# Optimization experiments

Hardware: AMD Instinct MI355X
Metric: run time of the kernel (lower is better)

Reference implementation:

```python
import jax, jax.numpy as jnp
import numpy as np

B, N, D, H = 8, 1024, 512, 512  # batch, nodes/graph, input dim, hidden/output dim
NEG_SLOPE = 0.2


def _gatv2_layer(x, src, dst, Wl, bl, Wr, br, a, bias, nseg):
    """PyG GATv2Conv (heads=1, add_self_loops=False, eval mode -> no dropout).
    message j->i: alpha_ij = softmax_i( a . leaky_relu(xl[j] + xr[i]) ); out[i] = sum_j alpha_ij * xl[j] + bias
    """
    xl = x @ Wl + bl              # [nseg, H] source transform
    xr = x @ Wr + br              # [nseg, H] target transform
    e = jax.nn.leaky_relu(xl[src] + xr[dst], NEG_SLOPE) @ a  # [E] raw scores
    m = jax.lax.stop_gradient(jax.ops.segment_max(e, dst, num_segments=nseg))
    ex = jnp.exp(e - m[dst])
    s = jax.ops.segment_sum(ex, dst, num_segments=nseg)
    alpha = ex / s[dst]                                       # segment softmax over incoming edges
    out = jax.ops.segment_sum(alpha[:, None] * xl[src], dst, num_segments=nseg)
    return out + bias


def setup_inputs() -> dict:
    key = jax.random.key(0)
    rng = np.random.RandomState(0)
    # random per-graph adjacency, avg degree ~16; block-diagonal edge extraction
    adj_np = (rng.rand(B, N, N) < (16.0 / N))
    srcs, dsts = [], []
    for b in range(B):  # matches torch.nonzero(big_adj).t(): row=src, col=dst
        r, c = np.nonzero(adj_np[b])
        srcs.append(r + b * N)
        dsts.append(c + b * N)
    edge_index = jnp.asarray(np.stack([np.concatenate(srcs), np.concatenate(dsts)]).astype(np.int32))

    ks = jax.random.split(key, 32)
    def lin(k, fi, fo):
        return (jax.random.normal(k, (fi, fo), jnp.float32) / np.sqrt(fi)).astype(jnp.float32)
    inp = {
        "batch_graph": jax.random.normal(ks[0], (B, N, D), jnp.float32),
        "adj": jnp.asarray(adj_np.astype(np.float32)),
        "edge_index": edge_index,
    }
    dims = [(D, H), (H, H), (H, H)]
    for i, (fi, fo) in enumerate(dims, start=1):
        k = jax.random.split(ks[i], 6)
        inp[f"Wl{i}"] = lin(k[0], fi, fo)
        inp[f"bl{i}"] = jnp.zeros((fo,), jnp.float32)
        inp[f"Wr{i}"] = lin(k[1], fi, fo)
        inp[f"br{i}"] = jnp.zeros((fo,), jnp.float32)
        inp[f"a{i}"] = (jax.random.normal(k[2], (fo,), jnp.float32) / np.sqrt(fo)).astype(jnp.float32)
        inp[f"bias{i}"] = jnp.zeros((fo,), jnp.float32)
    return inp


def reference(batch_graph, adj, edge_index,
              Wl1, bl1, Wr1, br1, a1, bias1,
              Wl2, bl2, Wr2, br2, a2, bias2,
              Wl3, bl3, Wr3, br3, a3, bias3):
    b, n, d = batch_graph.shape
    nseg = b * n
    x = batch_graph.reshape(nseg, d)
    src, dst = edge_index[0], edge_index[1]
    x = _gatv2_layer(x, src, dst, Wl1, bl1, Wr1, br1, a1, bias1, nseg)  # graph_norm = Identity
    x = _gatv2_layer(x, src, dst, Wl2, bl2, Wr2, br2, a2, bias2, nseg)
    x = _gatv2_layer(x, src, dst, Wl3, bl3, Wr3, br3, a3, bias3, nseg)
    return x.reshape(b, n, -1)
```

## Files before the change

### kernel.cpp

```cpp
#include <hip/hip_runtime.h>
#include <math.h>

#define MTOT 8192
#define HD   512

typedef __attribute__((ext_vector_type(8))) short bf16x8;
typedef __attribute__((ext_vector_type(4))) float floatx4;

__device__ inline unsigned short f2bf(float f) {
    unsigned int u = __float_as_uint(f);
    unsigned int r = (u + 0x7FFFu + ((u >> 16) & 1u)) >> 16;
    return (unsigned short)r;
}
__device__ inline float bf2f(unsigned short h) {
    return __uint_as_float(((unsigned int)h) << 16);
}


__global__ void count_deg(const int* __restrict__ dst, int* __restrict__ deg, int E) {
    int i = blockIdx.x * 256 + threadIdx.x;
    if (i < E) atomicAdd(&deg[dst[i]], 1);
}

__global__ __launch_bounds__(1024) void scan_offsets(const int* __restrict__ deg,
                                                     int* __restrict__ offs,
                                                     int* __restrict__ cursor) {
    __shared__ int part[1024];
    int tid = threadIdx.x;
    int base = tid * 8;
    int v[8]; int s = 0;
    #pragma unroll
    for (int i = 0; i < 8; ++i) { v[i] = deg[base + i]; s += v[i]; }
    part[tid] = s;
    __syncthreads();
    for (int off = 1; off < 1024; off <<= 1) {
        int t = (tid >= off) ? part[tid - off] : 0;
        __syncthreads();
        part[tid] += t;
        __syncthreads();
    }
    int run = (tid == 0) ? 0 : part[tid - 1];
    #pragma unroll
    for (int i = 0; i < 8; ++i) {
        offs[base + i] = run;
        cursor[base + i] = run;
        run += v[i];
    }
    if (tid == 1023) offs[MTOT] = run;
}

__global__ void scatter_edges(const int* __restrict__ src, const int* __restrict__ dst,
                              int* __restrict__ cursor, int* __restrict__ csr_src, int E) {
    int i = blockIdx.x * 256 + threadIdx.x;
    if (i < E) {
        int p = atomicAdd(&cursor[dst[i]], 1);
        csr_src[p] = src[i];
    }
}


__global__ __launch_bounds__(256) void prep_convert(
    const float* __restrict__ W0, const float* __restrict__ W1,
    const float* __restrict__ W2, const float* __restrict__ W3,
    const float* __restrict__ W4, const float* __restrict__ W5,
    unsigned short* __restrict__ wtbase,
    const float* __restrict__ X,
    unsigned short* __restrict__ Ahi, unsigned short* __restrict__ Alo,
    int* __restrict__ deg)
{
    int z = blockIdx.z;
    if (z == 7) {
        if (blockIdx.x == 0 && blockIdx.y == 0)
            for (int i = threadIdx.x; i < MTOT; i += 256) deg[i] = 0;
        return;
    }
    if (z == 6) {
        int bid = blockIdx.x * 16 + blockIdx.y;
        int t0 = bid * 256 + threadIdx.x;
        #pragma unroll
        for (int it = 0; it < 16; ++it) {
            int i = (t0 + it * 65536) * 4;
            float4 vv = *(const float4*)(X + i);
            ushort4 h, l;
            h.x = f2bf(vv.x); l.x = f2bf(vv.x - bf2f(h.x));
            h.y = f2bf(vv.y); l.y = f2bf(vv.y - bf2f(h.y));
            h.z = f2bf(vv.z); l.z = f2bf(vv.z - bf2f(h.z));
            h.w = f2bf(vv.w); l.w = f2bf(vv.w - bf2f(h.w));
            *(ushort4*)(Ahi + i) = h;
            *(ushort4*)(Alo + i) = l;
        }
        return;
    }
    const float* W = (z == 0) ? W0 : (z == 1) ? W1 : (z == 2) ? W2
                   : (z == 3) ? W3 : (z == 4) ? W4 : W5;
    int L = z >> 1, lr = z & 1;
    const size_t SZ = (size_t)HD * HD;
    unsigned short* Whi = wtbase + (L * 4 + lr * 2) * SZ;
    unsigned short* Wlo = Whi + SZ;

    __shared__ float t[32][33];
    int bx = blockIdx.x * 32;
    int by = blockIdx.y * 32;
    int tx = threadIdx.x & 31, ty = threadIdx.x >> 5;
    for (int i = ty; i < 32; i += 8)
        t[i][tx] = W[(size_t)(by + i) * HD + bx + tx];
    __syncthreads();
    for (int i = ty; i < 32; i += 8) {
        float vv = t[tx][i];
        unsigned short h = f2bf(vv);
        unsigned short l = f2bf(vv - bf2f(h));
        Whi[(size_t)(bx + i) * HD + by + tx] = h;
        Wlo[(size_t)(bx + i) * HD + by + tx] = l;
    }
}


__global__ __launch_bounds__(256) void gemm_mfma_dual(
    const unsigned short* __restrict__ Ahi, const unsigned short* __restrict__ Alo,
    const unsigned short* __restrict__ Bhi_l, const unsigned short* __restrict__ Blo_l,
    const unsigned short* __restrict__ Bhi_r, const unsigned short* __restrict__ Blo_r,
    const float* __restrict__ bias_l, const float* __restrict__ bias_r,
    float* __restrict__ Cl, float* __restrict__ Cr,
    const float* __restrict__ avec,
    float* __restrict__ slpart, float* __restrict__ srpart)
{
    const unsigned short* Bhi = blockIdx.z ? Bhi_r : Bhi_l;
    const unsigned short* Blo = blockIdx.z ? Blo_r : Blo_l;
    const float* bias         = blockIdx.z ? bias_r : bias_l;
    float* C                  = blockIdx.z ? Cr : Cl;
    float* spart              = blockIdx.z ? srpart : slpart;

    __shared__ __align__(16) unsigned short lds[4 * 128 * 32];

    int tid = threadIdx.x;
    int wave = tid >> 6, lane = tid & 63;
    int bm = blockIdx.y * 128, bn = blockIdx.x * 128;

    const unsigned short* gsrc[4] = {Ahi, Alo, Bhi, Blo};
    int rowbase[4] = {bm, bm, bn, bn};

    const unsigned short* gbase =
        gsrc[wave] + (size_t)(rowbase[wave] + (lane >> 2)) * 512 + (lane & 3) * 8;

    floatx4 acc[4][4] = {};

    int wm = wave & 1, wn = wave >> 1;
    int lr = lane & 15, lq = lane >> 4;

    for (int k0 = 0; k0 < 512; k0 += 32) {
        const unsigned short* g = gbase + k0;
        #pragma unroll
        for (int rg = 0; rg < 8; ++rg) {
            __builtin_amdgcn_global_load_lds(
                (const __attribute__((address_space(1))) unsigned int*)(g + (size_t)rg * 16 * 512),
                (__attribute__((address_space(3))) unsigned int*)(&lds[wave * 4096 + rg * 512]),
                16, 0, 0);
        }
        __syncthreads();

        bf16x8 ah[4], al[4], bh[4], bl_[4];
        #pragma unroll
        for (int i = 0; i < 4; ++i) {
            int mrow = wm * 64 + i * 16 + lr;
            ah[i]  = *(const bf16x8*)&lds[0 * 4096 + mrow * 32 + lq * 8];
            al[i]  = *(const bf16x8*)&lds[1 * 4096 + mrow * 32 + lq * 8];
            int nrow = wn * 64 + i * 16 + lr;
            bh[i]  = *(const bf16x8*)&lds[2 * 4096 + nrow * 32 + lq * 8];
            bl_[i] = *(const bf16x8*)&lds[3 * 4096 + nrow * 32 + lq * 8];
        }
        #pragma unroll
        for (int i = 0; i < 4; ++i)
            #pragma unroll
            for (int j = 0; j < 4; ++j) {
                acc[i][j] = __builtin_amdgcn_mfma_f32_16x16x32_bf16(ah[i], bh[j],  acc[i][j], 0, 0, 0);
                acc[i][j] = __builtin_amdgcn_mfma_f32_16x16x32_bf16(ah[i], bl_[j], acc[i][j], 0, 0, 0);
                acc[i][j] = __builtin_amdgcn_mfma_f32_16x16x32_bf16(al[i], bh[j],  acc[i][j], 0, 0, 0);
            }
        __syncthreads();
    }

    #pragma unroll
    for (int j = 0; j < 4; ++j) {
        int n = bn + wn * 64 + j * 16 + lr;
        float bv = bias[n];
        #pragma unroll
        for (int i = 0; i < 4; ++i) {
            int mbase = bm + wm * 64 + i * 16 + lq * 4;
            #pragma unroll
            for (int r = 0; r < 4; ++r)
                C[(size_t)(mbase + r) * 512 + n] = acc[i][j][r] + bv;
        }
    }

    {
        float aj[4], bj[4];
        #pragma unroll
        for (int j = 0; j < 4; ++j) {
            int n = bn + wn * 64 + j * 16 + lr;
            aj[j] = avec[n];
            bj[j] = bias[n];
        }
        float badd = fmaf(aj[0], bj[0], fmaf(aj[1], bj[1],
                     fmaf(aj[2], bj[2], aj[3] * bj[3])));
        #pragma unroll
        for (int i = 0; i < 4; ++i) {
            #pragma unroll
            for (int r = 0; r < 4; ++r) {
                float v = fmaf(aj[0], acc[i][0][r],
                          fmaf(aj[1], acc[i][1][r],
                          fmaf(aj[2], acc[i][2][r],
                          fmaf(aj[3], acc[i][3][r], badd))));
                v += __shfl_xor(v, 1, 64);
                v += __shfl_xor(v, 2, 64);
                v += __shfl_xor(v, 4, 64);
                v += __shfl_xor(v, 8, 64);
                if (lr == 0) {
                    int row = bm + wm * 64 + i * 16 + lq * 4 + r;
                    spart[(size_t)row * 8 + blockIdx.x * 2 + wn] = v;
                }
            }
        }
    }
}


__global__ __launch_bounds__(256) void gat_online(
    const float* __restrict__ xl, const float* __restrict__ xr,
    const float* __restrict__ slpart, const float* __restrict__ srpart,
    const float* __restrict__ avec, const float* __restrict__ bias,
    const int* __restrict__ offs, const int* __restrict__ csr_src,
    float* __restrict__ out, unsigned short* __restrict__ Ohi,
    unsigned short* __restrict__ Olo, int write_fp32)
{
    int gid = blockIdx.x;
    int wv = threadIdx.x >> 6, lane = threadIdx.x & 63;
    int node = ((gid & 7) << 10) + ((gid >> 3) << 2) + wv;

    int nb = offs[node], ne = offs[node + 1];

    size_t rowoff = (size_t)node * HD + lane * 8;
    float4 r0 = *(const float4*)(xr + rowoff);
    float4 r1 = *(const float4*)(xr + rowoff + 4);
    float4 av0 = *(const float4*)(avec + lane * 8);
    float4 av1 = *(const float4*)(avec + lane * 8 + 4);

    float4 sr0 = *(const float4*)(srpart + (size_t)node * 8);
    float4 sr1 = *(const float4*)(srpart + (size_t)node * 8 + 4);
    float sr = ((sr0.x + sr0.y) + (sr0.z + sr0.w)) + ((sr1.x + sr1.y) + (sr1.z + sr1.w));

    float m = -3.0e38f, s = 0.f;
    float4 acc0 = {0.f, 0.f, 0.f, 0.f}, acc1 = {0.f, 0.f, 0.f, 0.f};

    int p = nb;
    int jnx = 0;
    float4 nx0 = {0,0,0,0}, nx1 = {0,0,0,0}, nsl0 = {0,0,0,0}, nsl1 = {0,0,0,0};
    if (p < ne) {
        int j0 = __builtin_amdgcn_readfirstlane(csr_src[p]);
        const float* xp = xl + (size_t)j0 * HD + lane * 8;
        nx0 = *(const float4*)xp;
        nx1 = *(const float4*)(xp + 4);
        nsl0 = *(const float4*)(slpart + (size_t)j0 * 8);
        nsl1 = *(const float4*)(slpart + (size_t)j0 * 8 + 4);
    }
    if (p + 1 < ne) jnx = __builtin_amdgcn_readfirstlane(csr_src[p + 1]);

    while (p < ne) {
        float4 cx0 = nx0, cx1 = nx1;
        float slj = ((nsl0.x + nsl0.y) + (nsl0.z + nsl0.w)) +
                    ((nsl1.x + nsl1.y) + (nsl1.z + nsl1.w));

        int jpre = jnx;
        if (p + 2 < ne) jnx = __builtin_amdgcn_readfirstlane(csr_src[p + 2]);
        if (p + 1 < ne) {
            const float* xp = xl + (size_t)jpre * HD + lane * 8;
            nx0 = *(const float4*)xp;
            nx1 = *(const float4*)(xp + 4);
            nsl0 = *(const float4*)(slpart + (size_t)jpre * 8);
            nsl1 = *(const float4*)(slpart + (size_t)jpre * 8 + 4);
        }

        float t, pe = 0.f;
        t = cx0.x + r0.x; pe = fmaf(av0.x, fabsf(t), pe);
        t = cx0.y + r0.y; pe = fmaf(av0.y, fabsf(t), pe);
        t = cx0.z + r0.z; pe = fmaf(av0.z, fabsf(t), pe);
        t = cx0.w + r0.w; pe = fmaf(av0.w, fabsf(t), pe);
        t = cx1.x + r1.x; pe = fmaf(av1.x, fabsf(t), pe);
        t = cx1.y + r1.y; pe = fmaf(av1.y, fabsf(t), pe);
        t = cx1.z + r1.z; pe = fmaf(av1.z, fabsf(t), pe);
        t = cx1.w + r1.w; pe = fmaf(av1.w, fabsf(t), pe);
        pe += __shfl_xor(pe, 1, 64);
        pe += __shfl_xor(pe, 2, 64);
        pe += __shfl_xor(pe, 4, 64);
        pe += __shfl_xor(pe, 8, 64);
        pe += __shfl_xor(pe, 16, 64);
        pe += __shfl_xor(pe, 32, 64);

        float e = fmaf(0.4f, pe, 0.6f * (slj + sr));

        float w;
        if (e > m) {
            float sc = __expf(m - e);
            s *= sc;
            acc0.x *= sc; acc0.y *= sc; acc0.z *= sc; acc0.w *= sc;
            acc1.x *= sc; acc1.y *= sc; acc1.z *= sc; acc1.w *= sc;
            m = e; w = 1.f;
        } else {
            w = __expf(e - m);
        }
        s += w;
        acc0.x = fmaf(w, cx0.x, acc0.x);
        acc0.y = fmaf(w, cx0.y, acc0.y);
        acc0.z = fmaf(w, cx0.z, acc0.z);
        acc0.w = fmaf(w, cx0.w, acc0.w);
        acc1.x = fmaf(w, cx1.x, acc1.x);
        acc1.y = fmaf(w, cx1.y, acc1.y);
        acc1.z = fmaf(w, cx1.z, acc1.z);
        acc1.w = fmaf(w, cx1.w, acc1.w);
        ++p;
    }

    float inv = (s > 0.f) ? 1.f / s : 0.f;
    float4 b0 = *(const float4*)(bias + lane * 8);
    float4 b1 = *(const float4*)(bias + lane * 8 + 4);
    float4 o0, o1;
    o0.x = fmaf(acc0.x, inv, b0.x); o0.y = fmaf(acc0.y, inv, b0.y);
    o0.z = fmaf(acc0.z, inv, b0.z); o0.w = fmaf(acc0.w, inv, b0.w);
    o1.x = fmaf(acc1.x, inv, b1.x); o1.y = fmaf(acc1.y, inv, b1.y);
    o1.z = fmaf(acc1.z, inv, b1.z); o1.w = fmaf(acc1.w, inv, b1.w);

    if (write_fp32) {
        *(float4*)(out + rowoff) = o0;
        *(float4*)(out + rowoff + 4) = o1;
    } else {
        ushort4 h, lo;
        h.x = f2bf(o0.x); lo.x = f2bf(o0.x - bf2f(h.x));
        h.y = f2bf(o0.y); lo.y = f2bf(o0.y - bf2f(h.y));
        h.z = f2bf(o0.z); lo.z = f2bf(o0.z - bf2f(h.z));
        h.w = f2bf(o0.w); lo.w = f2bf(o0.w - bf2f(h.w));
        *(ushort4*)(Ohi + rowoff) = h;
        *(ushort4*)(Olo + rowoff) = lo;
        h.x = f2bf(o1.x); lo.x = f2bf(o1.x - bf2f(h.x));
        h.y = f2bf(o1.y); lo.y = f2bf(o1.y - bf2f(h.y));
        h.z = f2bf(o1.z); lo.z = f2bf(o1.z - bf2f(h.z));
        h.w = f2bf(o1.w); lo.w = f2bf(o1.w - bf2f(h.w));
        *(ushort4*)(Ohi + rowoff + 4) = h;
        *(ushort4*)(Olo + rowoff + 4) = lo;
    }
}


extern "C" void kernel_launch(void* const* d_in, const int* in_sizes, int n_in,
                              void* d_out, int out_size, void* d_ws, size_t ws_size,
                              hipStream_t stream) {
    const float* x0 = (const float*)d_in[0];
    const int* eidx = (const int*)d_in[2];
    int E = in_sizes[2] / 2;
    const int* esrc = eidx;
    const int* edst = eidx + E;

    const float* Wl[3] = {(const float*)d_in[3],  (const float*)d_in[9],  (const float*)d_in[15]};
    const float* bl[3] = {(const float*)d_in[4],  (const float*)d_in[10], (const float*)d_in[16]};
    const float* Wr[3] = {(const float*)d_in[5],  (const float*)d_in[11], (const float*)d_in[17]};
    const float* br[3] = {(const float*)d_in[6],  (const float*)d_in[12], (const float*)d_in[18]};
    const float* av[3] = {(const float*)d_in[7],  (const float*)d_in[13], (const float*)d_in[19]};
    const float* bs[3] = {(const float*)d_in[8],  (const float*)d_in[14], (const float*)d_in[20]};

    char* w = (char*)d_ws;
    unsigned short* Ahi = (unsigned short*)w; w += (size_t)MTOT * HD * 2;
    unsigned short* Alo = (unsigned short*)w; w += (size_t)MTOT * HD * 2;
    unsigned short* wtbase = (unsigned short*)w; w += 12 * (size_t)HD * HD * 2;
    float* xl = (float*)w; w += (size_t)MTOT * HD * 4;
    float* xr = (float*)w; w += (size_t)MTOT * HD * 4;
    int* deg    = (int*)w;
    int* offs   = deg + MTOT;
    int* cursor = offs + MTOT + 8;
    int* csr    = cursor + MTOT;
    float* slpart = (float*)(((uintptr_t)(csr + E) + 63) & ~(uintptr_t)63);
    float* srpart = slpart + (size_t)MTOT * 8;
    const size_t SZ = (size_t)HD * HD;

    prep_convert<<<dim3(16, 16, 8), 256, 0, stream>>>(
        Wl[0], Wr[0], Wl[1], Wr[1], Wl[2], Wr[2], wtbase, x0, Ahi, Alo, deg);
    count_deg<<<(E + 255) / 256, 256, 0, stream>>>(edst, deg, E);
    scan_offsets<<<1, 1024, 0, stream>>>(deg, offs, cursor);
    scatter_edges<<<(E + 255) / 256, 256, 0, stream>>>(esrc, edst, cursor, csr, E);

    dim3 ggrid(HD / 128, MTOT / 128, 2);
    for (int L = 0; L < 3; ++L) {
        gemm_mfma_dual<<<ggrid, 256, 0, stream>>>(Ahi, Alo,
            wtbase + (L * 4 + 0) * SZ, wtbase + (L * 4 + 1) * SZ,
            wtbase + (L * 4 + 2) * SZ, wtbase + (L * 4 + 3) * SZ,
            bl[L], br[L], xl, xr, av[L], slpart, srpart);
        int last = (L == 2);
        gat_online<<<MTOT / 4, 256, 0, stream>>>(xl, xr, slpart, srpart, av[L], bs[L],
                                                 offs, csr,
                                                 last ? (float*)d_out : nullptr,
                                                 last ? nullptr : Ahi,
                                                 last ? nullptr : Alo,
                                                 last);
    }
}
```

Before: 346.6 us.

## Process four edges per iteration and drop the GEMM-epilogue score partials

The online-softmax aggregation now gathers four source rows per iteration and batches their shuffle reductions and exp calls, so more memory loads are in flight per wave. The leaky-ReLU decomposition (precomputed linear part via per-row a·x partial sums written by the GEMM epilogue) is replaced by computing leaky_relu directly per element. This removes the extra epilogue reduction and partial-sum traffic from the GEMM, at the cost of more VALU work per edge. Padding edges beyond the degree are masked with a very negative score.

```diff
diff --git a/kernel.cpp b/kernel.cpp
--- a/kernel.cpp
+++ b/kernel.cpp
@@ -120,15 +120,12 @@
     const unsigned short* __restrict__ Bhi_l, const unsigned short* __restrict__ Blo_l,
     const unsigned short* __restrict__ Bhi_r, const unsigned short* __restrict__ Blo_r,
     const float* __restrict__ bias_l, const float* __restrict__ bias_r,
-    float* __restrict__ Cl, float* __restrict__ Cr,
-    const float* __restrict__ avec,
-    float* __restrict__ slpart, float* __restrict__ srpart)
+    float* __restrict__ Cl, float* __restrict__ Cr)
 {
     const unsigned short* Bhi = blockIdx.z ? Bhi_r : Bhi_l;
     const unsigned short* Blo = blockIdx.z ? Blo_r : Blo_l;
     const float* bias         = blockIdx.z ? bias_r : bias_l;
     float* C                  = blockIdx.z ? Cr : Cl;
-    float* spart              = blockIdx.z ? srpart : slpart;
 
     __shared__ __align__(16) unsigned short lds[4 * 128 * 32];
 
@@ -191,42 +188,24 @@
                 C[(size_t)(mbase + r) * 512 + n] = acc[i][j][r] + bv;
         }
     }
-
-    {
-        float aj[4], bj[4];
-        #pragma unroll
-        for (int j = 0; j < 4; ++j) {
-            int n = bn + wn * 64 + j * 16 + lr;
-            aj[j] = avec[n];
-            bj[j] = bias[n];
-        }
-        float badd = fmaf(aj[0], bj[0], fmaf(aj[1], bj[1],
-                     fmaf(aj[2], bj[2], aj[3] * bj[3])));
-        #pragma unroll
-        for (int i = 0; i < 4; ++i) {
-            #pragma unroll
-            for (int r = 0; r < 4; ++r) {
-                float v = fmaf(aj[0], acc[i][0][r],
-                          fmaf(aj[1], acc[i][1][r],
-                          fmaf(aj[2], acc[i][2][r],
-                          fmaf(aj[3], acc[i][3][r], badd))));
-                v += __shfl_xor(v, 1, 64);
-                v += __shfl_xor(v, 2, 64);
-                v += __shfl_xor(v, 4, 64);
-                v += __shfl_xor(v, 8, 64);
-                if (lr == 0) {
-                    int row = bm + wm * 64 + i * 16 + lq * 4 + r;
-                    spart[(size_t)row * 8 + blockIdx.x * 2 + wn] = v;
-                }
-            }
-        }
-    }
-}
-
+}
+
+
+#define EDGE_DOT8(pe, xa, xb)                                                  \
+    {                                                                          \
+        float t_, l_;                                                          \
+        t_ = xa.x + r0.x; l_ = fmaf(0.4f, fabsf(t_), 0.6f * t_); pe = fmaf(av0.x, l_, pe); \
+        t_ = xa.y + r0.y; l_ = fmaf(0.4f, fabsf(t_), 0.6f * t_); pe = fmaf(av0.y, l_, pe); \
+        t_ = xa.z + r0.z; l_ = fmaf(0.4f, fabsf(t_), 0.6f * t_); pe = fmaf(av0.z, l_, pe); \
+        t_ = xa.w + r0.w; l_ = fmaf(0.4f, fabsf(t_), 0.6f * t_); pe = fmaf(av0.w, l_, pe); \
+        t_ = xb.x + r1.x; l_ = fmaf(0.4f, fabsf(t_), 0.6f * t_); pe = fmaf(av1.x, l_, pe); \
+        t_ = xb.y + r1.y; l_ = fmaf(0.4f, fabsf(t_), 0.6f * t_); pe = fmaf(av1.y, l_, pe); \
+        t_ = xb.z + r1.z; l_ = fmaf(0.4f, fabsf(t_), 0.6f * t_); pe = fmaf(av1.z, l_, pe); \
+        t_ = xb.w + r1.w; l_ = fmaf(0.4f, fabsf(t_), 0.6f * t_); pe = fmaf(av1.w, l_, pe); \
+    }
 
 __global__ __launch_bounds__(256) void gat_online(
     const float* __restrict__ xl, const float* __restrict__ xr,
-    const float* __restrict__ slpart, const float* __restrict__ srpart,
     const float* __restrict__ avec, const float* __restrict__ bias,
     const int* __restrict__ offs, const int* __restrict__ csr_src,
     float* __restrict__ out, unsigned short* __restrict__ Ohi,
@@ -244,79 +223,83 @@
     float4 av0 = *(const float4*)(avec + lane * 8);
     float4 av1 = *(const float4*)(avec + lane * 8 + 4);
 
-    float4 sr0 = *(const float4*)(srpart + (size_t)node * 8);
-    float4 sr1 = *(const float4*)(srpart + (size_t)node * 8 + 4);
-    float sr = ((sr0.x + sr0.y) + (sr0.z + sr0.w)) + ((sr1.x + sr1.y) + (sr1.z + sr1.w));
-
     float m = -3.0e38f, s = 0.f;
     float4 acc0 = {0.f, 0.f, 0.f, 0.f}, acc1 = {0.f, 0.f, 0.f, 0.f};
 
     int p = nb;
-    int jnx = 0;
-    float4 nx0 = {0,0,0,0}, nx1 = {0,0,0,0}, nsl0 = {0,0,0,0}, nsl1 = {0,0,0,0};
+    int jc0 = 0, jc1 = 0, jc2 = 0, jc3 = 0;
     if (p < ne) {
-        int j0 = __builtin_amdgcn_readfirstlane(csr_src[p]);
-        const float* xp = xl + (size_t)j0 * HD + lane * 8;
-        nx0 = *(const float4*)xp;
-        nx1 = *(const float4*)(xp + 4);
-        nsl0 = *(const float4*)(slpart + (size_t)j0 * 8);
-        nsl1 = *(const float4*)(slpart + (size_t)j0 * 8 + 4);
-    }
-    if (p + 1 < ne) jnx = __builtin_amdgcn_readfirstlane(csr_src[p + 1]);
+        jc0 = csr_src[p];
+        jc1 = (p + 1 < ne) ? csr_src[p + 1] : jc0;
+        jc2 = (p + 2 < ne) ? csr_src[p + 2] : jc0;
+        jc3 = (p + 3 < ne) ? csr_src[p + 3] : jc0;
+    }
 
     while (p < ne) {
-        float4 cx0 = nx0, cx1 = nx1;
-        float slj = ((nsl0.x + nsl0.y) + (nsl0.z + nsl0.w)) +
-                    ((nsl1.x + nsl1.y) + (nsl1.z + nsl1.w));
-
-        int jpre = jnx;
-        if (p + 2 < ne) jnx = __builtin_amdgcn_readfirstlane(csr_src[p + 2]);
-        if (p + 1 < ne) {
-            const float* xp = xl + (size_t)jpre * HD + lane * 8;
-            nx0 = *(const float4*)xp;
-            nx1 = *(const float4*)(xp + 4);
-            nsl0 = *(const float4*)(slpart + (size_t)jpre * 8);
-            nsl1 = *(const float4*)(slpart + (size_t)jpre * 8 + 4);
-        }
-
-        float t, pe = 0.f;
-        t = cx0.x + r0.x; pe = fmaf(av0.x, fabsf(t), pe);
-        t = cx0.y + r0.y; pe = fmaf(av0.y, fabsf(t), pe);
-        t = cx0.z + r0.z; pe = fmaf(av0.z, fabsf(t), pe);
-        t = cx0.w + r0.w; pe = fmaf(av0.w, fabsf(t), pe);
-        t = cx1.x + r1.x; pe = fmaf(av1.x, fabsf(t), pe);
-        t = cx1.y + r1.y; pe = fmaf(av1.y, fabsf(t), pe);
-        t = cx1.z + r1.z; pe = fmaf(av1.z, fabsf(t), pe);
-        t = cx1.w + r1.w; pe = fmaf(av1.w, fabsf(t), pe);
-        pe += __shfl_xor(pe, 1, 64);
-        pe += __shfl_xor(pe, 2, 64);
-        pe += __shfl_xor(pe, 4, 64);
-        pe += __shfl_xor(pe, 8, 64);
-        pe += __shfl_xor(pe, 16, 64);
-        pe += __shfl_xor(pe, 32, 64);
-
-        float e = fmaf(0.4f, pe, 0.6f * (slj + sr));
-
-        float w;
-        if (e > m) {
-            float sc = __expf(m - e);
+        const float* xp0 = xl + (size_t)jc0 * HD + lane * 8;
+        const float* xp1 = xl + (size_t)jc1 * HD + lane * 8;
+        const float* xp2 = xl + (size_t)jc2 * HD + lane * 8;
+        const float* xp3 = xl + (size_t)jc3 * HD + lane * 8;
+        float4 xa0 = *(const float4*)xp0, xb0 = *(const float4*)(xp0 + 4);
+        float4 xa1 = *(const float4*)xp1, xb1 = *(const float4*)(xp1 + 4);
+        float4 xa2 = *(const float4*)xp2, xb2 = *(const float4*)(xp2 + 4);
+        float4 xa3 = *(const float4*)xp3, xb3 = *(const float4*)(xp3 + 4);
+
+        bool v1 = (p + 1 < ne), v2 = (p + 2 < ne), v3 = (p + 3 < ne);
+
+        int jn0 = jc0, jn1 = jc0, jn2 = jc0, jn3 = jc0;
+        int pn = p + 4;
+        if (pn < ne) {
+            jn0 = csr_src[pn];
+            jn1 = (pn + 1 < ne) ? csr_src[pn + 1] : jn0;
+            jn2 = (pn + 2 < ne) ? csr_src[pn + 2] : jn0;
+            jn3 = (pn + 3 < ne) ? csr_src[pn + 3] : jn0;
+        }
+
+        float pe0 = 0.f, pe1 = 0.f, pe2 = 0.f, pe3 = 0.f;
+        EDGE_DOT8(pe0, xa0, xb0);
+        EDGE_DOT8(pe1, xa1, xb1);
+        EDGE_DOT8(pe2, xa2, xb2);
+        EDGE_DOT8(pe3, xa3, xb3);
+
+        #pragma unroll
+        for (int off = 1; off < 64; off <<= 1) {
+            pe0 += __shfl_xor(pe0, off, 64);
+            pe1 += __shfl_xor(pe1, off, 64);
+            pe2 += __shfl_xor(pe2, off, 64);
+            pe3 += __shfl_xor(pe3, off, 64);
+        }
+
+        float e0 = pe0;
+        float e1 = v1 ? pe1 : -3.0e38f;
+        float e2 = v2 ? pe2 : -3.0e38f;
+        float e3 = v3 ? pe3 : -3.0e38f;
+
+        float bm = fmaxf(fmaxf(e0, e1), fmaxf(e2, e3));
+        if (bm > m) {
+            float sc = __expf(m - bm);
             s *= sc;
             acc0.x *= sc; acc0.y *= sc; acc0.z *= sc; acc0.w *= sc;
             acc1.x *= sc; acc1.y *= sc; acc1.z *= sc; acc1.w *= sc;
-            m = e; w = 1.f;
-        } else {
-            w = __expf(e - m);
-        }
-        s += w;
-        acc0.x = fmaf(w, cx0.x, acc0.x);
-        acc0.y = fmaf(w, cx0.y, acc0.y);
-        acc0.z = fmaf(w, cx0.z, acc0.z);
-        acc0.w = fmaf(w, cx0.w, acc0.w);
-        acc1.x = fmaf(w, cx1.x, acc1.x);
-        acc1.y = fmaf(w, cx1.y, acc1.y);
-        acc1.z = fmaf(w, cx1.z, acc1.z);
-        acc1.w = fmaf(w, cx1.w, acc1.w);
-        ++p;
+            m = bm;
+        }
+        float w0 = __expf(e0 - m);
+        float w1 = __expf(e1 - m);
+        float w2 = __expf(e2 - m);
+        float w3 = __expf(e3 - m);
+        s += (w0 + w1) + (w2 + w3);
+
+        acc0.x = fmaf(w0, xa0.x, fmaf(w1, xa1.x, fmaf(w2, xa2.x, fmaf(w3, xa3.x, acc0.x))));
+        acc0.y = fmaf(w0, xa0.y, fmaf(w1, xa1.y, fmaf(w2, xa2.y, fmaf(w3, xa3.y, acc0.y))));
+        acc0.z = fmaf(w0, xa0.z, fmaf(w1, xa1.z, fmaf(w2, xa2.z, fmaf(w3, xa3.z, acc0.z))));
+        acc0.w = fmaf(w0, xa0.w, fmaf(w1, xa1.w, fmaf(w2, xa2.w, fmaf(w3, xa3.w, acc0.w))));
+        acc1.x = fmaf(w0, xb0.x, fmaf(w1, xb1.x, fmaf(w2, xb2.x, fmaf(w3, xb3.x, acc1.x))));
+        acc1.y = fmaf(w0, xb0.y, fmaf(w1, xb1.y, fmaf(w2, xb2.y, fmaf(w3, xb3.y, acc1.y))));
+        acc1.z = fmaf(w0, xb0.z, fmaf(w1, xb1.z, fmaf(w2, xb2.z, fmaf(w3, xb3.z, acc1.z))));
+        acc1.w = fmaf(w0, xb0.w, fmaf(w1, xb1.w, fmaf(w2, xb2.w, fmaf(w3, xb3.w, acc1.w))));
+
+        jc0 = jn0; jc1 = jn1; jc2 = jn2; jc3 = jn3;
+        p += 4;
     }
 
     float inv = (s > 0.f) ? 1.f / s : 0.f;
@@ -375,8 +358,6 @@
     int* offs   = deg + MTOT;
     int* cursor = offs + MTOT + 8;
     int* csr    = cursor + MTOT;
-    float* slpart = (float*)(((uintptr_t)(csr + E) + 63) & ~(uintptr_t)63);
-    float* srpart = slpart + (size_t)MTOT * 8;
     const size_t SZ = (size_t)HD * HD;
 
     prep_convert<<<dim3(16, 16, 8), 256, 0, stream>>>(
@@ -390,10 +371,9 @@
         gemm_mfma_dual<<<ggrid, 256, 0, stream>>>(Ahi, Alo,
             wtbase + (L * 4 + 0) * SZ, wtbase + (L * 4 + 1) * SZ,
             wtbase + (L * 4 + 2) * SZ, wtbase + (L * 4 + 3) * SZ,
-            bl[L], br[L], xl, xr, av[L], slpart, srpart);
+            bl[L], br[L], xl, xr);
         int last = (L == 2);
-        gat_online<<<MTOT / 4, 256, 0, stream>>>(xl, xr, slpart, srpart, av[L], bs[L],
-                                                 offs, csr,
+        gat_online<<<MTOT / 4, 256, 0, stream>>>(xl, xr, av[L], bs[L], offs, csr,
                                                  last ? (float*)d_out : nullptr,
                                                  last ? nullptr : Ahi,
                                                  last ? nullptr : Alo,
```

Result: faster. 321.3 us (-7.3%).
